# Performance work log

Measured on AMD Instinct MI355X. Metric: run time of the kernel, lower is better.

The kernel has to match this reference:

```python
import jax, jax.numpy as jnp
import numpy as np

N_NODES = 100000
N_EDGES = 1600000
IN_C, HID_C, OUT_C = 64, 64, 32


def setup_inputs() -> dict:
    key = jax.random.key(0)
    ks = jax.random.split(key, 10)
    return {
        "x": jax.random.normal(ks[0], (N_NODES, IN_C), dtype=jnp.float32),
        "edge_index": jax.random.randint(ks[1], (2, N_EDGES), 0, N_NODES, dtype=jnp.int32),
        "W_l": jax.random.normal(ks[2], (IN_C, HID_C), dtype=jnp.float32) * 0.1,
        "W_r": jax.random.normal(ks[3], (IN_C, HID_C), dtype=jnp.float32) * 0.1,
        "b1": jax.random.normal(ks[4], (HID_C,), dtype=jnp.float32) * 0.1,
        "W_g": jax.random.normal(ks[5], (HID_C, OUT_C), dtype=jnp.float32) * 0.1,
        "att_src": jax.random.normal(ks[6], (OUT_C,), dtype=jnp.float32) * 0.1,
        "att_dst": jax.random.normal(ks[7], (OUT_C,), dtype=jnp.float32) * 0.1,
        "b2": jax.random.normal(ks[8], (OUT_C,), dtype=jnp.float32) * 0.1,
    }


def _gnn(x, edge_index, W_l, W_r, b1, W_g, att_src, att_dst, b2):
    n = x.shape[0]
    src, dst = edge_index[0], edge_index[1]

    # --- SAGEConv: mean neighbor aggregation + root transform ---
    deg = jax.ops.segment_sum(jnp.ones_like(src, dtype=x.dtype), dst, num_segments=n)
    agg = jax.ops.segment_sum(x[src], dst, num_segments=n)  # [N, IN_C]
    agg = agg / jnp.maximum(deg, 1.0)[:, None]
    h = agg @ W_l + b1 + x @ W_r
    h = jax.nn.relu(h)
    # dropout(p=0.5) is identity in eval mode

    # --- GATConv (heads=1), with self-loops (PyG default) ---
    loop = jnp.arange(n, dtype=src.dtype)
    s = jnp.concatenate([src, loop])
    d = jnp.concatenate([dst, loop])
    z = h @ W_g                      # [N, OUT_C]
    a_s = z @ att_src                # [N] per-node source score
    a_d = z @ att_dst                # [N] per-node dest score
    e = jax.nn.leaky_relu(a_s[s] + a_d[d], negative_slope=0.2)  # [E+N]
    # segment softmax over edges grouped by destination node
    m = jax.ops.segment_max(e, d, num_segments=n)
    ex = jnp.exp(e - m[d])
    denom = jax.ops.segment_sum(ex, d, num_segments=n)
    alpha = ex / denom[d]
    out = jax.ops.segment_sum(alpha[:, None] * z[s], d, num_segments=n) + b2

    return jax.nn.log_softmax(out, axis=1)


def reference(x, edge_index, W_l, W_r, b1, W_g, att_src, att_dst, b2):
    return _gnn(x, edge_index, W_l, W_r, b1, W_g, att_src, att_dst, b2)
```

## Files before the change

kernel.cpp:

```cpp
#include <hip/hip_runtime.h>
#include <cstdint>
#include <cstddef>


typedef unsigned short ushort_t;
typedef unsigned int uint_t;
typedef __attribute__((ext_vector_type(8))) short short8;
typedef __attribute__((ext_vector_type(4))) float f32x4;
typedef __attribute__((ext_vector_type(2))) float f32x2;

__device__ inline ushort_t f2bf(float f) {
    uint_t u = __float_as_uint(f);
    uint_t r = (u + 0x7fffu + ((u >> 16) & 1u)) >> 16;
    return (ushort_t)r;
}

#define PART_CHUNK 8192


__global__ __launch_bounds__(256) void k_pre(const float* __restrict__ x, ushort_t* __restrict__ xh,
                                             unsigned char* __restrict__ xq,
                                             const int* __restrict__ ei, int* __restrict__ tot,
                                             const float* __restrict__ Wl, const float* __restrict__ Wr,
                                             const float* __restrict__ Wg,
                                             ushort_t* __restrict__ Wlrt, ushort_t* __restrict__ Wgt,
                                             unsigned char* __restrict__ zq,
                                             int n4, int E, int NB, int N, int nchunk) {
    __shared__ int h[512];
    int bid = blockIdx.x, tid = threadIdx.x;
    int idx = bid * 256 + tid;
    if (idx < n4) {
        float4 v = ((const float4*)x)[idx];
        ushort4 o = { f2bf(v.x), f2bf(v.y), f2bf(v.z), f2bf(v.w) };
        ((ushort4*)xh)[idx] = o;
        int r = 0;
        r = __builtin_amdgcn_cvt_pk_fp8_f32(v.x, v.y, r, false);
        r = __builtin_amdgcn_cvt_pk_fp8_f32(v.z, v.w, r, true);
        ((uint_t*)xq)[idx] = (uint_t)r;
    }
    if (bid < nchunk) {
        for (int b = tid; b < NB; b += 256) h[b] = 0;
        __syncthreads();
        int b0 = bid * PART_CHUNK;
        int b1 = min(b0 + PART_CHUNK, E);
        for (int j = b0 + tid; j < b1; j += 256) atomicAdd(&h[ei[E + j] >> 8], 1);
        __syncthreads();
        for (int b = tid; b < NB; b += 256) if (h[b]) atomicAdd(&tot[b], h[b]);
    } else if (bid == nchunk) {
        if (tid < 16) ((uint_t*)(xq + (size_t)N * 64))[tid] = 0;
        if (tid < 8)  ((uint_t*)(zq + (size_t)N * 32))[tid] = 0;
    } else if (bid >= 512 && bid < 544) {
        int t = (bid - 512) * 256 + tid;
        int n = t >> 7, k = t & 127;
        float v = (k < 64) ? Wl[k * 64 + n] : Wr[(k - 64) * 64 + n];
        Wlrt[n * 128 + k] = f2bf(v);
        if (t < 32 * 64) {
            int n2 = t >> 6, k2 = t & 63;
            Wgt[n2 * 64 + k2] = f2bf(Wg[k2 * 32 + n2]);
        }
    }
}


__global__ __launch_bounds__(256) void k_scan(const int* __restrict__ tot, int* __restrict__ base,
                                              int* __restrict__ gofs, int* __restrict__ rowptr,
                                              int NB, int E, int N) {
    __shared__ int t[256];
    int tid = threadIdx.x;
    int v0 = (2 * tid < NB) ? tot[2 * tid] : 0;
    int v1 = (2 * tid + 1 < NB) ? tot[2 * tid + 1] : 0;
    t[tid] = v0 + v1;
    __syncthreads();
    for (int off = 1; off < 256; off <<= 1) {
        int u = (tid >= off) ? t[tid - off] : 0;
        __syncthreads();
        t[tid] += u;
        __syncthreads();
    }
    int pairExcl = (tid > 0) ? t[tid - 1] : 0;
    if (2 * tid < NB)     { base[2 * tid] = pairExcl;          gofs[2 * tid] = pairExcl; }
    if (2 * tid + 1 < NB) { base[2 * tid + 1] = pairExcl + v0; gofs[2 * tid + 1] = pairExcl + v0; }
    if (tid == 0) { rowptr[N] = E; base[NB] = E; }
}


__global__ __launch_bounds__(256) void k_part(const int* __restrict__ ei, int* __restrict__ gofs,
                                              uint_t* __restrict__ pairs, int E, int NB) {
    __shared__ int h[512];
    __shared__ int ofs[512];
    int tid = threadIdx.x;
    for (int b = tid; b < NB; b += 256) h[b] = 0;
    __syncthreads();
    int b0 = blockIdx.x * PART_CHUNK;
    int b1 = min(b0 + PART_CHUNK, E);
    for (int j = b0 + tid; j < b1; j += 256) atomicAdd(&h[ei[E + j] >> 8], 1);
    __syncthreads();
    for (int b = tid; b < NB; b += 256) ofs[b] = h[b] ? atomicAdd(&gofs[b], h[b]) : 0;
    __syncthreads();
    for (int j = b0 + tid; j < b1; j += 256) {
        int d = ei[E + j], s = ei[j];
        int p = atomicAdd(&ofs[d >> 8], 1);
        pairs[p] = (uint_t)s | ((uint_t)(d & 255) << 24);
    }
}


__global__ __launch_bounds__(256) void k_csr(const uint_t* __restrict__ pairs, const int* __restrict__ base,
                                             int* __restrict__ rowptr, int* __restrict__ csr, int N) {
    __shared__ int h[256];
    __shared__ int s[256];
    int b = blockIdx.x;
    int d0 = b << 8;
    int e0 = base[b], e1 = base[b + 1];
    int tid = threadIdx.x;
    h[tid] = 0;
    __syncthreads();
    for (int j = e0 + tid; j < e1; j += 256) atomicAdd(&h[pairs[j] >> 24], 1);
    __syncthreads();
    int v = h[tid];
    s[tid] = v;
    __syncthreads();
    for (int off = 1; off < 256; off <<= 1) {
        int u = (tid >= off) ? s[tid - off] : 0;
        __syncthreads();
        s[tid] += u;
        __syncthreads();
    }
    int excl = s[tid] - v;
    if (d0 + tid < N) rowptr[d0 + tid] = e0 + excl;
    __syncthreads();
    h[tid] = e0 + excl;
    __syncthreads();
    for (int j = e0 + tid; j < e1; j += 256) {
        uint_t p = pairs[j];
        int pos = atomicAdd(&h[p >> 24], 1);
        csr[pos] = (int)(p & 0xffffffu);
    }
}


__global__ __launch_bounds__(256) void k_gather(const int* __restrict__ rowptr, const int* __restrict__ csr,
                                                const unsigned char* __restrict__ xq,
                                                ushort_t* __restrict__ aggh, int N) {
    __shared__ int scr[256];
    int tid = threadIdx.x;
    int l = tid & 15, g = tid >> 4;
    int i = blockIdx.x * 16 + g;
    if (i >= N) return;
    int r0 = rowptr[i], r1 = rowptr[i + 1];
    const char* xb = (const char*)xq + l * 4;
    float a0 = 0.f, a1 = 0.f, a2 = 0.f, a3 = 0.f;
    for (int bb = r0; bb < r1; bb += 16) {
        int idx = bb + l;
        int src = (idx < r1) ? csr[idx] : N;
        scr[tid] = src << 6;
        #pragma unroll
        for (int r = 0; r < 4; ++r) {
            uint4 q = *(const uint4*)&scr[g * 16 + r * 4];
            #pragma unroll
            for (int e = 0; e < 4; ++e) {
                uint_t off = (e == 0) ? q.x : (e == 1) ? q.y : (e == 2) ? q.z : q.w;
                uint_t u = *(const uint_t*)(xb + off);
                f32x2 p0 = __builtin_amdgcn_cvt_pk_f32_fp8((int)u, false);
                f32x2 p1 = __builtin_amdgcn_cvt_pk_f32_fp8((int)u, true);
                a0 += p0.x; a1 += p0.y; a2 += p1.x; a3 += p1.y;
            }
        }
    }
    float dn = 1.0f / fmaxf((float)(r1 - r0), 1.0f);
    ushort4 o = { f2bf(a0 * dn), f2bf(a1 * dn), f2bf(a2 * dn), f2bf(a3 * dn) };
    *(ushort4*)(aggh + (size_t)i * 64 + l * 4) = o;
}


__global__ __launch_bounds__(256) void k_gemm(const ushort_t* __restrict__ aggh, const ushort_t* __restrict__ xh,
                                              const ushort_t* __restrict__ Wlrt, const ushort_t* __restrict__ Wgt,
                                              const float* __restrict__ b1,
                                              const float* __restrict__ att_src, const float* __restrict__ att_dst,
                                              unsigned char* __restrict__ zq, float* __restrict__ a_s,
                                              float* __restrict__ a_d, int N) {
    __shared__ ushort_t Wls[64 * 136];
    __shared__ ushort_t Wgs[32 * 72];
    __shared__ ushort_t hs[64 * 136];
    int tid = threadIdx.x;
    for (int t = tid; t < 64 * 16; t += 256) {
        int n = t >> 4, cq = t & 15;
        *(uint4*)(&Wls[n * 136 + cq * 8]) = *(const uint4*)(&Wlrt[n * 128 + cq * 8]);
    }
    for (int t = tid; t < 32 * 8; t += 256) {
        int n = t >> 3, cq = t & 7;
        *(uint4*)(&Wgs[n * 72 + cq * 8]) = *(const uint4*)(&Wgt[n * 64 + cq * 8]);
    }
    __syncthreads();

    int w = tid >> 6, lane = tid & 63;
    int c = lane & 15, quad = lane >> 4;
    int m0 = blockIdx.x * 64 + w * 16;
    int row = m0 + c;
    bool rowok = row < N;

    f32x4 acc[4] = {};
    #pragma unroll
    for (int kk = 0; kk < 4; ++kk) {
        const ushort_t* Abase = (kk < 2) ? aggh : xh;
        int koff = (kk & 1) * 32 + quad * 8;
        short8 a = {};
        if (rowok) a = *(const short8*)(Abase + (size_t)row * 64 + koff);
        #pragma unroll
        for (int nb = 0; nb < 4; ++nb) {
            short8 b = *(const short8*)(&Wls[(nb * 16 + c) * 136 + kk * 32 + quad * 8]);
            acc[nb] = __builtin_amdgcn_mfma_f32_16x16x32_bf16(a, b, acc[nb], 0, 0, 0);
        }
    }
    ushort_t* hw = &hs[w * 16 * 136];
    #pragma unroll
    for (int nb = 0; nb < 4; ++nb) {
        float bb = b1[nb * 16 + c];
        #pragma unroll
        for (int r = 0; r < 4; ++r) {
            float h = acc[nb][r] + bb;
            hw[(quad * 4 + r) * 136 + nb * 16 + c] = f2bf(fmaxf(h, 0.f));
        }
    }
    f32x4 acc2[2] = {};
    #pragma unroll
    for (int kk = 0; kk < 2; ++kk) {
        short8 a = *(const short8*)(&hw[c * 136 + kk * 32 + quad * 8]);
        #pragma unroll
        for (int nb = 0; nb < 2; ++nb) {
            short8 b = *(const short8*)(&Wgs[(nb * 16 + c) * 72 + kk * 32 + quad * 8]);
            acc2[nb] = __builtin_amdgcn_mfma_f32_16x16x32_bf16(a, b, acc2[nb], 0, 0, 0);
        }
    }
    float as0 = att_src[c], as1 = att_src[16 + c];
    float ad0 = att_dst[c], ad1 = att_dst[16 + c];
    #pragma unroll
    for (int r = 0; r < 4; ++r) {
        int grow = m0 + quad * 4 + r;
        float z0 = acc2[0][r], z1 = acc2[1][r];
        float ps = z0 * as0 + z1 * as1;
        float pd = z0 * ad0 + z1 * ad1;
        #pragma unroll
        for (int off = 8; off; off >>= 1) {
            ps += __shfl_xor(ps, off, 64);
            pd += __shfl_xor(pd, off, 64);
        }
        if (grow < N) {
            int r8 = __builtin_amdgcn_cvt_pk_fp8_f32(z0, z1, 0, false);
            unsigned char* zrow = zq + (size_t)grow * 32;
            zrow[c] = (unsigned char)(r8 & 0xff);
            zrow[16 + c] = (unsigned char)((r8 >> 8) & 0xff);
            if (c == 0) { a_s[grow] = ps; a_d[grow] = pd; }
        }
    }
}


__global__ __launch_bounds__(256) void k_gat(const unsigned char* __restrict__ zq, const float* __restrict__ a_s,
                                             const float* __restrict__ a_d, const int* __restrict__ rowptr,
                                             const int* __restrict__ csr, const float* __restrict__ b2,
                                             float* __restrict__ out, int N) {
    __shared__ uint2 scr[256];
    int tid = threadIdx.x;
    int l = tid & 15, g = tid >> 4;
    int i = blockIdx.x * 16 + g;
    if (i >= N) return;
    int r0 = rowptr[i], r1 = rowptr[i + 1];
    float adi = a_d[i], asi = a_s[i];
    const char* zb = (const char*)zq + l * 2;
    float accx = 0.f, accy = 0.f, dsum = 0.f;

    for (int bb = r0; bb < r1; bb += 16) {
        int idx = bb + l;
        bool valid = idx < r1;
        int s_l = valid ? csr[idx] : N;
        float w_l = 0.f;
        if (valid) {
            float e = a_s[s_l] + adi;
            e = fmaxf(e, 0.2f * e);
            w_l = __expf(e);
            dsum += w_l;
        }
        scr[tid] = make_uint2((uint_t)(s_l << 5), __float_as_uint(w_l));
        #pragma unroll
        for (int r = 0; r < 8; ++r) {
            uint4 q = *(const uint4*)&scr[g * 16 + r * 2];
            {
                uint_t u = *(const ushort_t*)(zb + q.x);
                f32x2 p = __builtin_amdgcn_cvt_pk_f32_fp8((int)u, false);
                float w = __uint_as_float(q.y);
                accx += w * p.x; accy += w * p.y;
            }
            {
                uint_t u = *(const ushort_t*)(zb + q.z);
                f32x2 p = __builtin_amdgcn_cvt_pk_f32_fp8((int)u, false);
                float w = __uint_as_float(q.w);
                accx += w * p.x; accy += w * p.y;
            }
        }
    }
    #pragma unroll
    for (int off = 8; off; off >>= 1) dsum += __shfl_xor(dsum, off, 64);
    float es = asi + adi; es = fmaxf(es, 0.2f * es);
    float wse = __expf(es);
    float denom = dsum + wse;
    uint_t us = *(const ushort_t*)((const char*)zq + (size_t)i * 32 + l * 2);
    f32x2 pself = __builtin_amdgcn_cvt_pk_f32_fp8((int)us, false);
    accx += wse * pself.x;
    accy += wse * pself.y;

    float rden = 1.0f / denom;
    float o0 = accx * rden + b2[l * 2];
    float o1 = accy * rden + b2[l * 2 + 1];
    float m2 = fmaxf(o0, o1);
    #pragma unroll
    for (int off = 8; off; off >>= 1) m2 = fmaxf(m2, __shfl_xor(m2, off, 64));
    float ssum = __expf(o0 - m2) + __expf(o1 - m2);
    #pragma unroll
    for (int off = 8; off; off >>= 1) ssum += __shfl_xor(ssum, off, 64);
    float lg = m2 + __logf(ssum);
    float2 r = { o0 - lg, o1 - lg };
    *(float2*)(out + (size_t)i * 32 + l * 2) = r;
}


extern "C" void kernel_launch(void* const* d_in, const int* in_sizes, int n_in,
                              void* d_out, int out_size, void* d_ws, size_t ws_size,
                              hipStream_t stream) {
    const float* x       = (const float*)d_in[0];
    const int*   ei      = (const int*)d_in[1];
    const float* Wl      = (const float*)d_in[2];
    const float* Wr      = (const float*)d_in[3];
    const float* b1      = (const float*)d_in[4];
    const float* Wg      = (const float*)d_in[5];
    const float* att_src = (const float*)d_in[6];
    const float* att_dst = (const float*)d_in[7];
    const float* b2      = (const float*)d_in[8];
    float* out = (float*)d_out;

    int N = in_sizes[0] / 64;
    int E = in_sizes[1] / 2;
    int NB = (N + 255) >> 8;

    char* ws = (char*)d_ws;
    size_t off = 0;
    auto alloc = [&](size_t bytes) { size_t r = off; off += (bytes + 255) & ~(size_t)255; return r; };
    int* tot       = (int*)(ws + alloc((size_t)(NB + 1) * 4));
    int* base      = (int*)(ws + alloc((size_t)(NB + 1) * 4));
    int* gofs      = (int*)(ws + alloc((size_t)(NB + 1) * 4));
    int* rowptr    = (int*)(ws + alloc((size_t)(N + 1) * 4));
    uint_t* pairs  = (uint_t*)(ws + alloc((size_t)E * 4));
    int* csr       = (int*)(ws + alloc((size_t)E * 4));
    ushort_t* xh   = (ushort_t*)(ws + alloc((size_t)N * 64 * 2));
    unsigned char* xq = (unsigned char*)(ws + alloc((size_t)(N + 1) * 64));
    ushort_t* aggh = (ushort_t*)(ws + alloc((size_t)N * 64 * 2));
    unsigned char* zq = (unsigned char*)(ws + alloc((size_t)(N + 1) * 32));
    float* a_s     = (float*)(ws + alloc((size_t)N * 4));
    float* a_d     = (float*)(ws + alloc((size_t)N * 4));
    ushort_t* Wlrt = (ushort_t*)(ws + alloc(64 * 128 * 2));
    ushort_t* Wgt  = (ushort_t*)(ws + alloc(32 * 64 * 2));

    (void)hipMemsetAsync(tot, 0, (size_t)NB * 4, stream);

    int nchunk = (E + PART_CHUNK - 1) / PART_CHUNK;
    int n4 = N * 64 / 4;
    int gpre = (n4 + 255) / 256;
    if (gpre < 545) gpre = 545;
    k_pre    <<<gpre, 256, 0, stream>>>(x, xh, xq, ei, tot, Wl, Wr, Wg, Wlrt, Wgt, zq, n4, E, NB, N, nchunk);
    k_scan   <<<1, 256, 0, stream>>>(tot, base, gofs, rowptr, NB, E, N);
    k_part   <<<nchunk, 256, 0, stream>>>(ei, gofs, pairs, E, NB);
    k_csr    <<<NB, 256, 0, stream>>>(pairs, base, rowptr, csr, N);
    k_gather <<<(N + 15) / 16, 256, 0, stream>>>(rowptr, csr, xq, aggh, N);
    k_gemm   <<<(N + 63) / 64, 256, 0, stream>>>(aggh, xh, Wlrt, Wgt, b1, att_src, att_dst, zq, a_s, a_d, N);
    k_gat    <<<(N + 15) / 16, 256, 0, stream>>>(zq, a_s, a_d, rowptr, csr, b2, out, N);
}
```

Baseline: 206.7 us.

## Split gather into two 32-byte column halves with half-group edge interleave

The fp8 neighbor gather now makes two passes over each node's edge list, each covering 32 of the 64 feature bytes. Within a 16-lane group, two 8-lane sub-groups take alternate edges, and their partial sums are combined with a cross-lane shuffle. The goal is to change the memory access shape so each wavefront touches 32-byte segments from more rows at once, which may improve gather coalescing or parallelism. The cost is reading the CSR indices twice and doing extra shuffles. The partition chunk size used for edge bucketing is also doubled.

```diff
diff --git a/kernel.cpp b/kernel.cpp
--- a/kernel.cpp
+++ b/kernel.cpp
@@ -15,7 +15,7 @@
     return (ushort_t)r;
 }
 
-#define PART_CHUNK 8192
+#define PART_CHUNK 16384
 
 
 __global__ __launch_bounds__(256) void k_pre(const float* __restrict__ x, ushort_t* __restrict__ xh,
@@ -148,28 +148,42 @@
     int i = blockIdx.x * 16 + g;
     if (i >= N) return;
     int r0 = rowptr[i], r1 = rowptr[i + 1];
-    const char* xb = (const char*)xq + l * 4;
-    float a0 = 0.f, a1 = 0.f, a2 = 0.f, a3 = 0.f;
-    for (int bb = r0; bb < r1; bb += 16) {
-        int idx = bb + l;
-        int src = (idx < r1) ? csr[idx] : N;
-        scr[tid] = src << 6;
-        #pragma unroll
-        for (int r = 0; r < 4; ++r) {
-            uint4 q = *(const uint4*)&scr[g * 16 + r * 4];
-            #pragma unroll
-            for (int e = 0; e < 4; ++e) {
-                uint_t off = (e == 0) ? q.x : (e == 1) ? q.y : (e == 2) ? q.z : q.w;
-                uint_t u = *(const uint_t*)(xb + off);
-                f32x2 p0 = __builtin_amdgcn_cvt_pk_f32_fp8((int)u, false);
-                f32x2 p1 = __builtin_amdgcn_cvt_pk_f32_fp8((int)u, true);
-                a0 += p0.x; a1 += p0.y; a2 += p1.x; a3 += p1.y;
-            }
-        }
-    }
+    int sub = l >> 3, lc = l & 7;
     float dn = 1.0f / fmaxf((float)(r1 - r0), 1.0f);
-    ushort4 o = { f2bf(a0 * dn), f2bf(a1 * dn), f2bf(a2 * dn), f2bf(a3 * dn) };
-    *(ushort4*)(aggh + (size_t)i * 64 + l * 4) = o;
+
+    #pragma unroll
+    for (int p = 0; p < 2; ++p) {
+        const char* xb = (const char*)xq + p * 32 + lc * 4;
+        float a0 = 0.f, a1 = 0.f, a2 = 0.f, a3 = 0.f;
+        for (int bb = r0; bb < r1; bb += 16) {
+            int idx = bb + l;
+            int src = (idx < r1) ? csr[idx] : N;
+            scr[tid] = src << 6;
+            uint4 q0 = *(const uint4*)&scr[g * 16 + 0];
+            uint4 q1 = *(const uint4*)&scr[g * 16 + 4];
+            uint4 q2 = *(const uint4*)&scr[g * 16 + 8];
+            uint4 q3 = *(const uint4*)&scr[g * 16 + 12];
+#define HSTEP(oa, ob) { \
+            uint_t off = sub ? (ob) : (oa); \
+            uint_t u = *(const uint_t*)(xb + off); \
+            f32x2 p0 = __builtin_amdgcn_cvt_pk_f32_fp8((int)u, false); \
+            f32x2 p1 = __builtin_amdgcn_cvt_pk_f32_fp8((int)u, true); \
+            a0 += p0.x; a1 += p0.y; a2 += p1.x; a3 += p1.y; }
+            HSTEP(q0.x, q0.y) HSTEP(q0.z, q0.w)
+            HSTEP(q1.x, q1.y) HSTEP(q1.z, q1.w)
+            HSTEP(q2.x, q2.y) HSTEP(q2.z, q2.w)
+            HSTEP(q3.x, q3.y) HSTEP(q3.z, q3.w)
+#undef HSTEP
+        }
+        a0 += __shfl_xor(a0, 8, 64);
+        a1 += __shfl_xor(a1, 8, 64);
+        a2 += __shfl_xor(a2, 8, 64);
+        a3 += __shfl_xor(a3, 8, 64);
+        if (sub == 0) {
+            ushort4 o = { f2bf(a0 * dn), f2bf(a1 * dn), f2bf(a2 * dn), f2bf(a3 * dn) };
+            *(ushort4*)(aggh + (size_t)i * 64 + p * 32 + lc * 4) = o;
+        }
+    }
 }
 
 
```

Measured after the change: 225.0 us. 1.09x slower.
